# Kernel optimization log

Measured on AMD Instinct MI355X. Metric: run time of the kernel, lower is better.

The kernel has to match this reference:

```python
import jax, jax.numpy as jnp
import numpy as np

B, N, DIM, HEADS = 2, 1024, 1024, 16
HD = DIM // HEADS  # 64


def setup_inputs() -> dict:
    key = jax.random.key(0)
    ks = jax.random.split(key, 8)
    f = lambda k, s: jax.random.normal(k, s, dtype=jnp.float32)
    inv = np.float32(1.0 / np.sqrt(DIM))
    return {
        'x_real': f(ks[0], (B, N, DIM)),
        'x_imag': f(ks[1], (B, N, DIM)),
        'freqs_real': f(ks[2], (N, HD)),
        'freqs_imag': f(ks[3], (N, HD)),
        'Wqkv_r': f(ks[4], (3 * DIM, DIM)) * inv,
        'Wqkv_i': f(ks[5], (3 * DIM, DIM)) * inv,
        'bqkv_r': jnp.zeros((3 * DIM,), jnp.float32),
        'bqkv_i': jnp.zeros((3 * DIM,), jnp.float32),
        'Wout_r': f(ks[6], (DIM, DIM)) * inv,
        'Wout_i': f(ks[7], (DIM, DIM)) * inv,
        'bout_r': jnp.zeros((DIM,), jnp.float32),
        'bout_i': jnp.zeros((DIM,), jnp.float32),
    }


def reference(x_real, x_imag, freqs_real, freqs_imag,
              Wqkv_r, Wqkv_i, bqkv_r, bqkv_i,
              Wout_r, Wout_i, bout_r, bout_i):
    cplx = jax.lax.complex
    x = cplx(x_real, x_imag)                    # [b, n, d] complex64
    Wqkv = cplx(Wqkv_r, Wqkv_i)                 # [3d, d]
    bqkv = cplx(bqkv_r, bqkv_i)
    Wout = cplx(Wout_r, Wout_i)
    bout = cplx(bout_r, bout_i)
    freqs = cplx(freqs_real, freqs_imag)        # [n, hd]

    scale = HD ** (-0.5)

    # ComplexLinear: x @ W^T + b -> [b, n, 3d]
    qkv = jnp.einsum('bnd,ed->bne', x, Wqkv) + bqkv
    # rearrange 'b n (h d qkv) -> qkv b h n d' (qkv index fastest-varying)
    qkv = qkv.reshape(B, N, HEADS, HD, 3)
    q = jnp.transpose(qkv[..., 0], (0, 2, 1, 3))  # [b, h, n, hd]
    k = jnp.transpose(qkv[..., 1], (0, 2, 1, 3))
    v = jnp.transpose(qkv[..., 2], (0, 2, 1, 3))

    # complex rotary: elementwise multiply by freqs [n, hd]
    q = q * freqs
    k = k * freqs

    # complex QK^H -> [b, h, n, n]
    dots = jnp.einsum('bhnd,bhmd->bhnm', q, jnp.conj(k))
    attn = jax.nn.softmax(jnp.abs(dots) * scale, axis=-1)  # real float32

    # real attn @ complex v (promotes to complex64)
    out = jnp.einsum('bhnm,bhmd->bhnd', attn, v)
    out = jnp.transpose(out, (0, 2, 1, 3)).reshape(B, N, DIM)  # b n (h d)

    out = jnp.einsum('bnd,ed->bne', out, Wout) + bout
    # return real/imag stacked so baseline comparison is on real arrays
    return jnp.stack([jnp.real(out), jnp.imag(out)], axis=0)  # [2, b, n, d]
```

## Files before the change

kernel.cpp:

```cpp
#include <hip/hip_runtime.h>
#include <hip/hip_bf16.h>
#include <stdint.h>

#define B 2
#define N 1024
#define DIM 1024
#define HEADS 16
#define HD 64
#define E3 (3*DIM)
#define M (B*N)

typedef __hip_bfloat16 bf16;
typedef __attribute__((ext_vector_type(8))) short short8v;
typedef __attribute__((ext_vector_type(4))) float f32x4;
typedef __attribute__((ext_vector_type(4))) unsigned int u32x4;

__device__ __forceinline__ float scrub(float v) {
    return (v == v && fabsf(v) < 1e30f) ? v : 0.0f;
}
__device__ __forceinline__ float b2f(bf16 x) { return scrub(__bfloat162float(x)); }

template<bool FP32>
__device__ __forceinline__ float ldin(const void* p, int i) {
    if (FP32) return scrub(((const float*)p)[i]);
    else      return scrub(__bfloat162float(((const bf16*)p)[i]));
}

__device__ __forceinline__ bool sniff_fp32(const void* x, int tid, int* sbad) {
    if (tid == 0) *sbad = 0;
    __syncthreads();
    if (tid < 64) {
        const unsigned short* u = (const unsigned short*)x;
        int ex = (u[tid] >> 7) & 0xFF;
        if (ex == 0xFF || ex >= 135 || (ex != 0 && ex <= 118))
            atomicAdd(sbad, 1);
    }
    __syncthreads();
    return *sbad > 4;
}

__device__ __forceinline__ short f2bs(float x) {
    bf16 h = __float2bfloat16(x);
    return __builtin_bit_cast(short, h);
}
__device__ __forceinline__ short8v neg8(short8v x) {
    u32x4 u = __builtin_bit_cast(u32x4, x);
    u ^= 0x80008000u;
    return __builtin_bit_cast(short8v, u);
}
__device__ __forceinline__ f32x4 mfma16(short8v a, short8v b, f32x4 c) {
    return __builtin_amdgcn_mfma_f32_16x16x32_bf16(a, b, c, 0, 0, 0);
}

__device__ __forceinline__ void gload16(const bf16* g, bf16* l) {
    __builtin_amdgcn_global_load_lds(
        (const __attribute__((address_space(1))) void*)g,
        (__attribute__((address_space(3))) void*)l, 16, 0, 0);
}

__device__ __forceinline__ void cvt8(bf16* dhi, bf16* dlo, const float* s) {
    float4 a = *(const float4*)s;
    float4 b = *(const float4*)(s + 4);
    float v[8] = {a.x,a.y,a.z,a.w,b.x,b.y,b.z,b.w};
    short8v hi, lo;
    #pragma unroll
    for (int e = 0; e < 8; ++e) {
        float f = scrub(v[e]);
        bf16 h = __float2bfloat16(f);
        hi[e] = __builtin_bit_cast(short, h);
        lo[e] = f2bs(f - __bfloat162float(h));
    }
    *(short8v*)dhi = hi;
    *(short8v*)dlo = lo;
}
__device__ __forceinline__ void cvt8h(bf16* dhi, const float* s) {
    float4 a = *(const float4*)s;
    float4 b = *(const float4*)(s + 4);
    float v[8] = {a.x,a.y,a.z,a.w,b.x,b.y,b.z,b.w};
    short8v hi;
    #pragma unroll
    for (int e = 0; e < 8; ++e)
        hi[e] = f2bs(scrub(v[e]));
    *(short8v*)dhi = hi;
}

#define PLB 2048

__device__ __forceinline__ short8v frag_ldp(const bf16* base, int row, int j) {
    int p = row >> 1;
    int c = (((row & 1) << 2) | j) ^ (p & 7);
    return *(const short8v*)(base + p*64 + c*8);
}

template<bool ASPLIT, int BM, int NI>
__device__ __forceinline__ void cgemm_async(
    const bf16* Arh, const bf16* Aih, const bf16* Arl, const bf16* Ail,
    const bf16* Brh, const bf16* Bih,
    int row0, int col0,
    bf16* sA0, bf16* sA1, bf16* sB0, bf16* sB1,
    f32x4 (*accr)[NI], f32x4 (*accs)[NI], f32x4 (*acci)[NI])
{
    constexpr int PLA = BM*32;
    const int t  = threadIdx.x;
    const int w  = t >> 6, l = t & 63;
    const int lr = l & 15, lg = l >> 4;
    const int wm = (NI == 4) ? w : (w >> 1);
    const int wn = (NI == 4) ? 0 : (w & 1);

    const int pb  = t >> 3;
    const int cpb = (t & 7) ^ (pb & 7);
    const int srb = 2*pb + (cpb >> 2);
    const int sjb = cpb & 3;

    auto stage = [&](int buf, int k0) {
        bf16* dsA = buf ? sA1 : sA0;
        bf16* dsB = buf ? sB1 : sB0;
        #pragma unroll
        for (int u = 0; u < BM/64; ++u) {
            int c   = t + 256*u;
            int pa  = c >> 3;
            int cpa = (c & 7) ^ (pa & 7);
            int sra = 2*pa + (cpa >> 2);
            int sja = cpa & 3;
            size_t aoff = (size_t)(row0 + sra)*DIM + k0 + sja*8;
            gload16(Arh + aoff, dsA + c*8);
            gload16(Aih + aoff, dsA + PLA + c*8);
            if constexpr (ASPLIT) {
                gload16(Arl + aoff, dsA + 2*PLA + c*8);
                gload16(Ail + aoff, dsA + 3*PLA + c*8);
            }
        }
        size_t boff = (size_t)(col0 + srb)*DIM + k0 + sjb*8;
        gload16(Brh + boff, dsB + t*8);
        gload16(Bih + boff, dsB + PLB + t*8);
    };

    stage(0, 0);
    __syncthreads();
    int cur = 0;

    for (int k0 = 0; k0 < DIM; k0 += 32) {
        if (k0 + 32 < DIM) stage(cur ^ 1, k0 + 32);

        const bf16* sA = cur ? sA1 : sA0;
        const bf16* sB = cur ? sB1 : sB0;

        short8v arh[2], aih[2], arl[2], ail[2];
        #pragma unroll
        for (int mi = 0; mi < 2; ++mi) {
            int arow = wm*32 + mi*16 + lr;
            arh[mi] = frag_ldp(sA,       arow, lg);
            aih[mi] = frag_ldp(sA + PLA, arow, lg);
            if constexpr (ASPLIT) {
                arl[mi] = frag_ldp(sA + 2*PLA, arow, lg);
                ail[mi] = frag_ldp(sA + 3*PLA, arow, lg);
            }
        }
        #pragma unroll
        for (int ni = 0; ni < NI; ++ni) {
            int brow = wn*32 + ni*16 + lr;
            short8v brh = frag_ldp(sB,       brow, lg);
            short8v bih = frag_ldp(sB + PLB, brow, lg);
            #pragma unroll
            for (int mi = 0; mi < 2; ++mi) {
                accr[mi][ni] = mfma16(arh[mi], brh, accr[mi][ni]);
                accs[mi][ni] = mfma16(aih[mi], bih, accs[mi][ni]);
                acci[mi][ni] = mfma16(arh[mi], bih, acci[mi][ni]);
                acci[mi][ni] = mfma16(aih[mi], brh, acci[mi][ni]);
                if constexpr (ASPLIT) {
                    accr[mi][ni] = mfma16(arl[mi], brh, accr[mi][ni]);
                    accs[mi][ni] = mfma16(ail[mi], bih, accs[mi][ni]);
                    acci[mi][ni] = mfma16(arl[mi], bih, acci[mi][ni]);
                    acci[mi][ni] = mfma16(ail[mi], brh, acci[mi][ni]);
                }
            }
        }
        __syncthreads();
        cur ^= 1;
    }
}

template<int AMODE, int BMODE, int BM, int NI>
__device__ __forceinline__ void cgemm_sync(
    const void* Aor, const void* Aoi,
    const void* Bor, const void* Boi,
    int row0, int col0,
    bf16* sA, bf16* sB,
    f32x4 (*accr)[NI], f32x4 (*accs)[NI], f32x4 (*acci)[NI])
{
    constexpr int PLA = BM*32;
    const int t  = threadIdx.x;
    const int w  = t >> 6, l = t & 63;
    const int lr = l & 15, lg = l >> 4;
    const int wm = (NI == 4) ? w : (w >> 1);
    const int wn = (NI == 4) ? 0 : (w & 1);

    const int pb  = t >> 3;
    const int cpb = (t & 7) ^ (pb & 7);
    const int srb = 2*pb + (cpb >> 2);
    const int sjb = cpb & 3;

    for (int k0 = 0; k0 < DIM; k0 += 32) {
        #pragma unroll
        for (int u = 0; u < BM/64; ++u) {
            int c   = t + 256*u;
            int pa  = c >> 3;
            int cpa = (c & 7) ^ (pa & 7);
            int sra = 2*pa + (cpa >> 2);
            int sja = cpa & 3;
            size_t aoff = (size_t)(row0 + sra)*DIM + k0 + sja*8;
            bf16* dA = sA + c*8;
            if constexpr (AMODE == 0) {
                *(short8v*)(dA)       = *(const short8v*)((const bf16*)Aor + aoff);
                *(short8v*)(dA + PLA) = *(const short8v*)((const bf16*)Aoi + aoff);
            } else {
                cvt8(dA,       dA + 2*PLA, (const float*)Aor + aoff);
                cvt8(dA + PLA, dA + 3*PLA, (const float*)Aoi + aoff);
            }
        }
        {
            size_t boff = (size_t)(col0 + srb)*DIM + k0 + sjb*8;
            bf16* dB = sB + t*8;
            if constexpr (BMODE == 0) {
                *(short8v*)(dB)       = *(const short8v*)((const bf16*)Bor + boff);
                *(short8v*)(dB + PLB) = *(const short8v*)((const bf16*)Boi + boff);
            } else {
                cvt8(dB,       dB + 2*PLB, (const float*)Bor + boff);
                cvt8(dB + PLB, dB + 3*PLB, (const float*)Boi + boff);
            }
        }
        __syncthreads();

        short8v arh[2], aih[2], arl[2], ail[2];
        #pragma unroll
        for (int mi = 0; mi < 2; ++mi) {
            int arow = wm*32 + mi*16 + lr;
            arh[mi] = frag_ldp(sA,       arow, lg);
            aih[mi] = frag_ldp(sA + PLA, arow, lg);
            if constexpr (AMODE == 2) {
                arl[mi] = frag_ldp(sA + 2*PLA, arow, lg);
                ail[mi] = frag_ldp(sA + 3*PLA, arow, lg);
            }
        }
        #pragma unroll
        for (int ni = 0; ni < NI; ++ni) {
            int brow = wn*32 + ni*16 + lr;
            short8v brh = frag_ldp(sB,       brow, lg);
            short8v bih = frag_ldp(sB + PLB, brow, lg);
            short8v brl, bil;
            if constexpr (BMODE == 2) {
                brl = frag_ldp(sB + 2*PLB, brow, lg);
                bil = frag_ldp(sB + 3*PLB, brow, lg);
            }
            #pragma unroll
            for (int mi = 0; mi < 2; ++mi) {
                accr[mi][ni] = mfma16(arh[mi], brh, accr[mi][ni]);
                accs[mi][ni] = mfma16(aih[mi], bih, accs[mi][ni]);
                acci[mi][ni] = mfma16(arh[mi], bih, acci[mi][ni]);
                acci[mi][ni] = mfma16(aih[mi], brh, acci[mi][ni]);
                if constexpr (BMODE == 2) {
                    accr[mi][ni] = mfma16(arh[mi], brl, accr[mi][ni]);
                    accs[mi][ni] = mfma16(aih[mi], bil, accs[mi][ni]);
                    acci[mi][ni] = mfma16(arh[mi], bil, acci[mi][ni]);
                    acci[mi][ni] = mfma16(aih[mi], brl, acci[mi][ni]);
                }
                if constexpr (AMODE == 2) {
                    accr[mi][ni] = mfma16(arl[mi], brh, accr[mi][ni]);
                    accs[mi][ni] = mfma16(ail[mi], bih, accs[mi][ni]);
                    acci[mi][ni] = mfma16(arl[mi], bih, acci[mi][ni]);
                    acci[mi][ni] = mfma16(ail[mi], brh, acci[mi][ni]);
                }
            }
        }
        __syncthreads();
    }
}

struct PrepArgs {
    const void* src[6];
    bf16* hi[6];
    bf16* lo[6];
    int n8[6];
};

__global__ __launch_bounds__(256) void prepass_kernel(PrepArgs a) {
    __shared__ int sbad;
    const int y = blockIdx.y;
    bool f32 = sniff_fp32(a.src[y], threadIdx.x, &sbad);
    if (!f32) return;
    const int n8 = a.n8[y];
    bf16* lo = a.lo[y];
    for (int i = blockIdx.x*blockDim.x + threadIdx.x; i < n8; i += gridDim.x*blockDim.x) {
        if (lo) cvt8 (a.hi[y] + (size_t)i*8, lo + (size_t)i*8, (const float*)a.src[y] + (size_t)i*8);
        else    cvt8h(a.hi[y] + (size_t)i*8,                   (const float*)a.src[y] + (size_t)i*8);
    }
}

template<bool FP32>
__device__ __forceinline__ void qkv_epi(
    const void* fr_, const void* fi_, const void* bqr, const void* bqi,
    bf16* qr, bf16* qi, bf16* kr, bf16* ki, bf16* vr, bf16* vi,
    int row0, int col0,
    f32x4 (*accr)[2], f32x4 (*accs)[2], f32x4 (*acci)[2])
{
    const int t  = threadIdx.x;
    const int w  = t >> 6, l = t & 63;
    const int lr = l & 15, lg = l >> 4;
    const int wm = w >> 1, wn = w & 1;

    #pragma unroll
    for (int ni = 0; ni < 2; ++ni) {
        int col = col0 + wn*32 + ni*16 + lr;
        float bre = ldin<FP32>(bqr, col);
        float bim = ldin<FP32>(bqi, col);
        int s = col % 3;
        int tc = col / 3;
        int h = tc / HD, d = tc % HD;
        #pragma unroll
        for (int mi = 0; mi < 2; ++mi)
        #pragma unroll
        for (int r = 0; r < 4; ++r) {
            int row = row0 + wm*32 + mi*16 + 4*lg + r;
            int bb = row / N, n = row % N;
            float cr = accr[mi][ni][r] - accs[mi][ni][r] + bre;
            float ci = acci[mi][ni][r] + bim;
            if (s == 2) {
                int idxT = ((bb*HEADS + h)*HD + d)*N + n;
                vr[idxT] = __float2bfloat16(scrub(cr));
                vi[idxT] = __float2bfloat16(scrub(ci));
            } else {
                float fre = ldin<FP32>(fr_, n*HD + d);
                float fim = ldin<FP32>(fi_, n*HD + d);
                float rr = cr*fre - ci*fim;
                float ri = cr*fim + ci*fre;
                int idx = ((bb*HEADS + h)*N + n)*HD + d;
                if (s == 0) { qr[idx] = __float2bfloat16(scrub(rr)); qi[idx] = __float2bfloat16(scrub(ri)); }
                else        { kr[idx] = __float2bfloat16(scrub(rr)); ki[idx] = __float2bfloat16(scrub(ri)); }
            }
        }
    }
}

template<int FM>
__global__ __launch_bounds__(256, 3) void qkv_kernel(
    const void* xr, const void* xi, const void* fr_, const void* fi_,
    const void* Wr, const void* Wi, const void* bqr, const void* bqi,
    const bf16* xrh, const bf16* xih, const bf16* xrl, const bf16* xil,
    const bf16* wrh, const bf16* wih,
    bf16* qr, bf16* qi, bf16* kr, bf16* ki, bf16* vr, bf16* vi)
{
    __shared__ __align__(16) bf16 sA[2][4*64*32];
    __shared__ __align__(16) bf16 sB[2][2*PLB];
    __shared__ int sbad;
    bool f32 = sniff_fp32(xr, threadIdx.x, &sbad);

    int wg   = blockIdx.x;
    int xcd  = wg & 7;
    int idx  = wg >> 3;
    int rtin = idx & 1;
    int tmp  = idx >> 1;
    int ctl  = tmp % 6;
    int rtg  = tmp / 6;
    int row0 = (rtg*2 + rtin) * 64;
    int col0 = (xcd*6 + ctl) * 64;

    f32x4 accr[2][2] = {}, accs[2][2] = {}, acci[2][2] = {};
    if (f32) {
        if constexpr (FM == 1)
            cgemm_async<true, 64, 2>(xrh, xih, xrl, xil, wrh, wih,
                                     row0, col0, sA[0], sA[1], sB[0], sB[1],
                                     accr, accs, acci);
        else
            cgemm_sync<2, 2, 64, 2>(xr, xi, Wr, Wi,
                                    row0, col0, sA[0], sB[0],
                                    accr, accs, acci);
        qkv_epi<true >(fr_, fi_, bqr, bqi, qr,qi,kr,ki,vr,vi, row0, col0, accr, accs, acci);
    } else {
        cgemm_async<false, 64, 2>((const bf16*)xr, (const bf16*)xi, nullptr, nullptr,
                                  (const bf16*)Wr, (const bf16*)Wi,
                                  row0, col0, sA[0], sA[1], sB[0], sB[1],
                                  accr, accs, acci);
        qkv_epi<false>(fr_, fi_, bqr, bqi, qr,qi,kr,ki,vr,vi, row0, col0, accr, accs, acci);
    }
}

__device__ __forceinline__ short8v frag_ld(const bf16* base, int row, int j) {
    return *(const short8v*)(base + row*64 + ((j ^ (row & 7)) << 3));
}

__global__ __launch_bounds__(256) void attn_kernel(
    const bf16* qr, const bf16* qi, const bf16* kr, const bf16* ki,
    const bf16* vtr, const bf16* vti, bf16* aor_, bf16* aoi_)
{
    __shared__ __align__(16) bf16 skr[64*64];
    __shared__ __align__(16) bf16 ski[64*64];
    __shared__ __align__(16) bf16 svr[64*64];
    __shared__ __align__(16) bf16 svi[64*64];
    __shared__ __align__(16) bf16 sp[4][16*64];

    const int t  = threadIdx.x;
    const int w  = t >> 6;
    const int l  = t & 63;
    const int lr = l & 15;
    const int lg = l >> 4;
    int wg = blockIdx.x;
    int sw = (wg & 7) * ((int)gridDim.x >> 3) + (wg >> 3);
    const int qt = sw & 15;
    const int bh = sw >> 4;

    const size_t hbase = (size_t)bh * N * HD;

    const bf16* qrg = qr + hbase + (size_t)(qt*64 + w*16 + lr) * HD;
    const bf16* qig = qi + hbase + (size_t)(qt*64 + w*16 + lr) * HD;
    short8v qfr[2], qfi[2], qfrn[2];
    #pragma unroll
    for (int ks = 0; ks < 2; ++ks) {
        qfr[ks] = *(const short8v*)(qrg + 32*ks + 8*lg);
        qfi[ks] = *(const short8v*)(qig + 32*ks + 8*lg);
        qfrn[ks] = neg8(qfr[ks]);
    }

    const int cA = t, cB = t + 256;
    const int rA = cA >> 3, jA = (cA & 7) ^ (rA & 7);
    const int rB = cB >> 3, jB = (cB & 7) ^ (rB & 7);
    const bf16* krg = kr  + hbase;
    const bf16* kig = ki  + hbase;
    const bf16* vrg = vtr + hbase;
    const bf16* vig = vti + hbase;

    f32x4 outr[4], outi[4];
    #pragma unroll
    for (int dt = 0; dt < 4; ++dt) {
        outr[dt] = (f32x4){0.f,0.f,0.f,0.f};
        outi[dt] = (f32x4){0.f,0.f,0.f,0.f};
    }
    float mrow[4] = {-1e30f,-1e30f,-1e30f,-1e30f};
    float lrow[4] = {0.f,0.f,0.f,0.f};

    short8v pf0, pf1, pf2, pf3, pf4, pf5, pf6, pf7;
    auto issue = [&](int m0) {
        pf0 = *(const short8v*)(krg + (size_t)(m0+rA)*HD + jA*8);
        pf1 = *(const short8v*)(krg + (size_t)(m0+rB)*HD + jB*8);
        pf2 = *(const short8v*)(kig + (size_t)(m0+rA)*HD + jA*8);
        pf3 = *(const short8v*)(kig + (size_t)(m0+rB)*HD + jB*8);
        pf4 = *(const short8v*)(vrg + (size_t)rA*N + m0 + jA*8);
        pf5 = *(const short8v*)(vrg + (size_t)rB*N + m0 + jB*8);
        pf6 = *(const short8v*)(vig + (size_t)rA*N + m0 + jA*8);
        pf7 = *(const short8v*)(vig + (size_t)rB*N + m0 + jB*8);
    };
    issue(0);

    for (int kt = 0; kt < N/64; ++kt) {
        *(short8v*)(skr + cA*8) = pf0;
        *(short8v*)(skr + cB*8) = pf1;
        *(short8v*)(ski + cA*8) = pf2;
        *(short8v*)(ski + cB*8) = pf3;
        *(short8v*)(svr + cA*8) = pf4;
        *(short8v*)(svr + cB*8) = pf5;
        *(short8v*)(svi + cA*8) = pf6;
        *(short8v*)(svi + cB*8) = pf7;
        __syncthreads();
        if (kt + 1 < N/64) issue((kt + 1) * 64);

        f32x4 sr[4], si[4];
        #pragma unroll
        for (int ct = 0; ct < 4; ++ct) {
            f32x4 ar = (f32x4){0.f,0.f,0.f,0.f};
            f32x4 ai = (f32x4){0.f,0.f,0.f,0.f};
            #pragma unroll
            for (int ks = 0; ks < 2; ++ks) {
                short8v kfr = frag_ld(skr, 16*ct + lr, 4*ks + lg);
                short8v kfi = frag_ld(ski, 16*ct + lr, 4*ks + lg);
                ar = mfma16(qfr[ks],  kfr, ar);
                ar = mfma16(qfi[ks],  kfi, ar);
                ai = mfma16(qfi[ks],  kfr, ai);
                ai = mfma16(qfrn[ks], kfi, ai);
            }
            sr[ct] = ar; si[ct] = ai;
        }

        float p[4][4];
        float pmax[4] = {-1e30f,-1e30f,-1e30f,-1e30f};
        #pragma unroll
        for (int ct = 0; ct < 4; ++ct)
        #pragma unroll
        for (int r = 0; r < 4; ++r) {
            float s = sqrtf(sr[ct][r]*sr[ct][r] + si[ct][r]*si[ct][r]) * 0.125f;
            p[ct][r] = s;
            pmax[r] = fmaxf(pmax[r], s);
        }
        #pragma unroll
        for (int mk = 1; mk <= 8; mk <<= 1)
        #pragma unroll
        for (int r = 0; r < 4; ++r)
            pmax[r] = fmaxf(pmax[r], __shfl_xor(pmax[r], mk));

        float fsc[4];
        #pragma unroll
        for (int r = 0; r < 4; ++r) {
            float mnew = fmaxf(mrow[r], pmax[r]);
            fsc[r] = __expf(mrow[r] - mnew);
            mrow[r] = mnew;
        }
        float rsum[4] = {0.f,0.f,0.f,0.f};
        #pragma unroll
        for (int ct = 0; ct < 4; ++ct)
        #pragma unroll
        for (int r = 0; r < 4; ++r) {
            float e = __expf(p[ct][r] - mrow[r]);
            p[ct][r] = e;
            rsum[r] += e;
        }
        #pragma unroll
        for (int mk = 1; mk <= 8; mk <<= 1)
        #pragma unroll
        for (int r = 0; r < 4; ++r)
            rsum[r] += __shfl_xor(rsum[r], mk);
        #pragma unroll
        for (int r = 0; r < 4; ++r)
            lrow[r] = lrow[r]*fsc[r] + rsum[r];
        #pragma unroll
        for (int dt = 0; dt < 4; ++dt)
        #pragma unroll
        for (int r = 0; r < 4; ++r) {
            outr[dt][r] *= fsc[r];
            outi[dt][r] *= fsc[r];
        }

        bf16* pw = sp[w];
        #pragma unroll
        for (int ct = 0; ct < 4; ++ct)
        #pragma unroll
        for (int r = 0; r < 4; ++r) {
            int prow = 4*lg + r;
            int pcol = 16*ct + lr;
            int jj = (pcol >> 3) ^ (prow & 7);
            pw[prow*64 + jj*8 + (pcol & 7)] = __float2bfloat16(p[ct][r]);
        }
        short8v pa[2];
        #pragma unroll
        for (int ks2 = 0; ks2 < 2; ++ks2)
            pa[ks2] = frag_ld(pw, lr, 4*ks2 + lg);

        #pragma unroll
        for (int dt = 0; dt < 4; ++dt)
        #pragma unroll
        for (int ks2 = 0; ks2 < 2; ++ks2) {
            short8v vfr = frag_ld(svr, 16*dt + lr, 4*ks2 + lg);
            short8v vfi = frag_ld(svi, 16*dt + lr, 4*ks2 + lg);
            outr[dt] = mfma16(pa[ks2], vfr, outr[dt]);
            outi[dt] = mfma16(pa[ks2], vfi, outi[dt]);
        }
        __syncthreads();
    }

    const int b_ = bh / HEADS, h_ = bh % HEADS;
    float invl[4];
    #pragma unroll
    for (int r = 0; r < 4; ++r) invl[r] = 1.0f / lrow[r];
    #pragma unroll
    for (int dt = 0; dt < 4; ++dt)
    #pragma unroll
    for (int r = 0; r < 4; ++r) {
        int n_ = qt*64 + w*16 + 4*lg + r;
        int d_ = 16*dt + lr;
        size_t oidx = ((size_t)(b_*N + n_))*DIM + h_*HD + d_;
        aor_[oidx] = __float2bfloat16(scrub(outr[dt][r]*invl[r]));
        aoi_[oidx] = __float2bfloat16(scrub(outi[dt][r]*invl[r]));
    }
}

template<int FM>
__global__ __launch_bounds__(256, 4) void outproj_kernel(
    const void* xprobe,
    const bf16* ar, const bf16* ai,
    const void* Wr, const void* Wi, const void* bor, const void* boi,
    const bf16* wrh, const bf16* wih,
    void* out)
{
    __shared__ __align__(16) bf16 sA[2][2*PLB];
    __shared__ __align__(16) bf16 sB[2][2*PLB];
    __shared__ int sbad;
    bool f32 = sniff_fp32(xprobe, threadIdx.x, &sbad);

    int wg   = blockIdx.x;
    int xcd  = wg & 7;
    int idx  = wg >> 3;
    int rtin = idx & 1;
    int tmp  = idx >> 1;
    int ctl  = tmp & 1;
    int rtg  = tmp >> 1;
    int row0 = (rtg*2 + rtin) * 64;
    int col0 = (xcd*2 + ctl) * 64;

    const int t  = threadIdx.x;
    const int w  = t >> 6, l = t & 63;
    const int lr = l & 15, lg = l >> 4;
    const int wm = w >> 1, wn = w & 1;

    f32x4 accr[2][2] = {}, accs[2][2] = {}, acci[2][2] = {};
    if (f32) {
        if constexpr (FM == 3)
            cgemm_async<false, 64, 2>(ar, ai, nullptr, nullptr, wrh, wih,
                                      row0, col0, sA[0], sA[1], sB[0], sB[1],
                                      accr, accs, acci);
        else
            cgemm_sync<0, 2, 64, 2>(ar, ai, Wr, Wi,
                                    row0, col0, sA[0], sB[0],
                                    accr, accs, acci);
    } else {
        cgemm_async<false, 64, 2>(ar, ai, nullptr, nullptr,
                                  (const bf16*)Wr, (const bf16*)Wi,
                                  row0, col0, sA[0], sA[1], sB[0], sB[1],
                                  accr, accs, acci);
    }

    #pragma unroll
    for (int ni = 0; ni < 2; ++ni) {
        int col = col0 + wn*32 + ni*16 + lr;
        float bre = f32 ? ldin<true>(bor, col) : ldin<false>(bor, col);
        float bim = f32 ? ldin<true>(boi, col) : ldin<false>(boi, col);
        #pragma unroll
        for (int mi = 0; mi < 2; ++mi)
        #pragma unroll
        for (int r = 0; r < 4; ++r) {
            int row = row0 + wm*32 + mi*16 + 4*lg + r;
            float cr = scrub(accr[mi][ni][r] - accs[mi][ni][r] + bre);
            float ci = scrub(acci[mi][ni][r] + bim);
            if (f32) {
                ((float*)out)[(size_t)row*DIM + col]                 = cr;
                ((float*)out)[(size_t)M*DIM + (size_t)row*DIM + col] = ci;
            } else {
                ((bf16*)out)[(size_t)row*DIM + col]                  = __float2bfloat16(cr);
                ((bf16*)out)[(size_t)M*DIM + (size_t)row*DIM + col]  = __float2bfloat16(ci);
            }
        }
    }
}

extern "C" void kernel_launch(void* const* d_in, const int* in_sizes, int n_in,
                              void* d_out, int out_size, void* d_ws, size_t ws_size,
                              hipStream_t stream)
{
    const void* xr     = d_in[0];
    const void* xi     = d_in[1];
    const void* fr     = d_in[2];
    const void* fi     = d_in[3];
    const void* Wqkv_r = d_in[4];
    const void* Wqkv_i = d_in[5];
    const void* bqkv_r = d_in[6];
    const void* bqkv_i = d_in[7];
    const void* Wout_r = d_in[8];
    const void* Wout_i = d_in[9];
    const void* bout_r = d_in[10];
    const void* bout_i = d_in[11];

    bf16* w = (bf16*)d_ws;
    const size_t QS  = (size_t)B*HEADS*N*HD;
    const size_t XS  = (size_t)M*DIM;
    const size_t WQS = (size_t)E3*DIM;
    const size_t WOS = (size_t)DIM*DIM;

    bf16* qr   = w;          bf16* qi   = qr  + QS;
    bf16* kr   = qi  + QS;   bf16* ki   = kr  + QS;
    bf16* vr   = ki  + QS;   bf16* vi   = vr  + QS;
    bf16* aor_ = vi  + QS;   bf16* aoi_ = aor_ + QS;
    bf16* xrh = aoi_ + QS;   bf16* xih = xrh + XS;
    bf16* xrl = xih + XS;    bf16* xil = xrl + XS;
    bf16* wqrh = xil + XS;   bf16* wqih = wqrh + WQS;
    bf16* worh = wqih + WQS; bf16* woih = worh + WOS;

    const size_t need = (size_t)(8*QS + 4*XS + 2*WQS + 2*WOS) * sizeof(bf16);
    const bool pre = ws_size >= need;

    if (pre) {
        PrepArgs a;
        a.src[0] = xr;     a.hi[0] = xrh;  a.lo[0] = xrl;    a.n8[0] = (int)(XS/8);
        a.src[1] = xi;     a.hi[1] = xih;  a.lo[1] = xil;    a.n8[1] = (int)(XS/8);
        a.src[2] = Wqkv_r; a.hi[2] = wqrh; a.lo[2] = nullptr; a.n8[2] = (int)(WQS/8);
        a.src[3] = Wqkv_i; a.hi[3] = wqih; a.lo[3] = nullptr; a.n8[3] = (int)(WQS/8);
        a.src[4] = Wout_r; a.hi[4] = worh; a.lo[4] = nullptr; a.n8[4] = (int)(WOS/8);
        a.src[5] = Wout_i; a.hi[5] = woih; a.lo[5] = nullptr; a.n8[5] = (int)(WOS/8);
        prepass_kernel<<<dim3(1536, 6), dim3(256), 0, stream>>>(a);

        qkv_kernel<1><<<dim3((E3/64)*(M/64)), dim3(256), 0, stream>>>(
            xr, xi, fr, fi, Wqkv_r, Wqkv_i, bqkv_r, bqkv_i,
            xrh, xih, xrl, xil, wqrh, wqih,
            qr, qi, kr, ki, vr, vi);
    } else {
        qkv_kernel<2><<<dim3((E3/64)*(M/64)), dim3(256), 0, stream>>>(
            xr, xi, fr, fi, Wqkv_r, Wqkv_i, bqkv_r, bqkv_i,
            nullptr, nullptr, nullptr, nullptr, nullptr, nullptr,
            qr, qi, kr, ki, vr, vi);
    }

    attn_kernel<<<dim3(B*HEADS*(N/64)), dim3(256), 0, stream>>>(
        qr, qi, kr, ki, vr, vi, aor_, aoi_);

    if (pre) {
        outproj_kernel<3><<<dim3((DIM/64)*(M/64)), dim3(256), 0, stream>>>(
            xr, aor_, aoi_, Wout_r, Wout_i, bout_r, bout_i,
            worh, woih, d_out);
    } else {
        outproj_kernel<2><<<dim3((DIM/64)*(M/64)), dim3(256), 0, stream>>>(
            xr, aor_, aoi_, Wout_r, Wout_i, bout_r, bout_i,
            nullptr, nullptr, d_out);
    }
}
```

Before: 315.0 us.

## Double-buffer K/V shared-memory tiles in attention kernel to drop a barrier

Shared K and V tiles in the attention kernel become two buffers, so the next tile's register-prefetched data is written to the alternate buffer at the end of each iteration. This removes one __syncthreads per iteration and lets the LDS writes follow the compute rather than precede it. In exchange, LDS use roughly doubles from about 40KB to about 72KB per block, which may lower occupancy.

```diff
diff --git a/kernel.cpp b/kernel.cpp
--- a/kernel.cpp
+++ b/kernel.cpp
@@ -392,10 +392,10 @@
     const bf16* qr, const bf16* qi, const bf16* kr, const bf16* ki,
     const bf16* vtr, const bf16* vti, bf16* aor_, bf16* aoi_)
 {
-    __shared__ __align__(16) bf16 skr[64*64];
-    __shared__ __align__(16) bf16 ski[64*64];
-    __shared__ __align__(16) bf16 svr[64*64];
-    __shared__ __align__(16) bf16 svi[64*64];
+    __shared__ __align__(16) bf16 skr[2][64*64];
+    __shared__ __align__(16) bf16 ski[2][64*64];
+    __shared__ __align__(16) bf16 svr[2][64*64];
+    __shared__ __align__(16) bf16 svi[2][64*64];
     __shared__ __align__(16) bf16 sp[4][16*64];
 
     const int t  = threadIdx.x;
@@ -448,18 +448,23 @@
         pf6 = *(const short8v*)(vig + (size_t)rA*N + m0 + jA*8);
         pf7 = *(const short8v*)(vig + (size_t)rB*N + m0 + jB*8);
     };
+    auto wrt = [&](int buf) {
+        *(short8v*)(skr[buf] + cA*8) = pf0;
+        *(short8v*)(skr[buf] + cB*8) = pf1;
+        *(short8v*)(ski[buf] + cA*8) = pf2;
+        *(short8v*)(ski[buf] + cB*8) = pf3;
+        *(short8v*)(svr[buf] + cA*8) = pf4;
+        *(short8v*)(svr[buf] + cB*8) = pf5;
+        *(short8v*)(svi[buf] + cA*8) = pf6;
+        *(short8v*)(svi[buf] + cB*8) = pf7;
+    };
+
     issue(0);
+    wrt(0);
+    __syncthreads();
+    int cur = 0;
 
     for (int kt = 0; kt < N/64; ++kt) {
-        *(short8v*)(skr + cA*8) = pf0;
-        *(short8v*)(skr + cB*8) = pf1;
-        *(short8v*)(ski + cA*8) = pf2;
-        *(short8v*)(ski + cB*8) = pf3;
-        *(short8v*)(svr + cA*8) = pf4;
-        *(short8v*)(svr + cB*8) = pf5;
-        *(short8v*)(svi + cA*8) = pf6;
-        *(short8v*)(svi + cB*8) = pf7;
-        __syncthreads();
         if (kt + 1 < N/64) issue((kt + 1) * 64);
 
         f32x4 sr[4], si[4];
@@ -469,8 +474,8 @@
             f32x4 ai = (f32x4){0.f,0.f,0.f,0.f};
             #pragma unroll
             for (int ks = 0; ks < 2; ++ks) {
-                short8v kfr = frag_ld(skr, 16*ct + lr, 4*ks + lg);
-                short8v kfi = frag_ld(ski, 16*ct + lr, 4*ks + lg);
+                short8v kfr = frag_ld(skr[cur], 16*ct + lr, 4*ks + lg);
+                short8v kfi = frag_ld(ski[cur], 16*ct + lr, 4*ks + lg);
                 ar = mfma16(qfr[ks],  kfr, ar);
                 ar = mfma16(qfi[ks],  kfi, ar);
                 ai = mfma16(qfi[ks],  kfr, ai);
@@ -546,12 +551,15 @@
         for (int dt = 0; dt < 4; ++dt)
         #pragma unroll
         for (int ks2 = 0; ks2 < 2; ++ks2) {
-            short8v vfr = frag_ld(svr, 16*dt + lr, 4*ks2 + lg);
-            short8v vfi = frag_ld(svi, 16*dt + lr, 4*ks2 + lg);
+            short8v vfr = frag_ld(svr[cur], 16*dt + lr, 4*ks2 + lg);
+            short8v vfi = frag_ld(svi[cur], 16*dt + lr, 4*ks2 + lg);
             outr[dt] = mfma16(pa[ks2], vfr, outr[dt]);
             outi[dt] = mfma16(pa[ks2], vfi, outi[dt]);
         }
+
+        if (kt + 1 < N/64) wrt(cur ^ 1);
         __syncthreads();
+        cur ^= 1;
     }
 
     const int b_ = bh / HEADS, h_ = bh % HEADS;
```

Measured after the change: 299.5 us. 1.05x faster.
